# Kernel optimization log

Measured on AMD Instinct MI355X. Metric: run time of the kernel, lower is better.

Reference implementation:

```python
import jax, jax.numpy as jnp
import numpy as np
from jax import lax

S, B, VIN, VOUT, U, E = 64, 256, 128, 128, 1024, 512
START_CODE = 0
T_DEC = 25  # MAX_DECODE_STEPS


def gru_step(x, h, Wih, Whh, bih, bhh):
    # PyTorch GRU cell, gate order r,z,n
    gi = x @ Wih.T + bih
    gh = h @ Whh.T + bhh
    ir, iz, inn = jnp.split(gi, 3, axis=-1)
    hr, hz, hn = jnp.split(gh, 3, axis=-1)
    r = jax.nn.sigmoid(ir + hr)
    z = jax.nn.sigmoid(iz + hz)
    n = jnp.tanh(inn + r * hn)
    return (1.0 - z) * n + z * h


def setup_inputs() -> dict:
    key = jax.random.key(0)
    ks = jax.random.split(key, 20)
    sc = 0.05
    inp = {
        'x': jax.random.normal(ks[0], (S, B, VIN), jnp.float32),
        'x_len': jnp.maximum(jnp.sort(jax.random.randint(ks[1], (B,), 0, S + 1)), 1),
        'enc_Wih': jax.random.normal(ks[2], (3 * U, VIN), jnp.float32) * sc,
        'enc_Whh': jax.random.normal(ks[3], (3 * U, U), jnp.float32) * sc,
        'enc_bih': jnp.zeros((3 * U,), jnp.float32),
        'enc_bhh': jnp.zeros((3 * U,), jnp.float32),
        'dec_Wih': jax.random.normal(ks[4], (3 * U, E + U), jnp.float32) * sc,
        'dec_Whh': jax.random.normal(ks[5], (3 * U, U), jnp.float32) * sc,
        'dec_bih': jnp.zeros((3 * U,), jnp.float32),
        'dec_bhh': jnp.zeros((3 * U,), jnp.float32),
        'o2h_W': jax.random.normal(ks[6], (E, VOUT), jnp.float32) * sc,
        'o2h_b': jnp.zeros((E,), jnp.float32),
        'fc_W': jax.random.normal(ks[7], (VOUT, U), jnp.float32) * sc,
        'fc_b': jnp.zeros((VOUT,), jnp.float32),
        'W1_W': jax.random.normal(ks[8], (U, U), jnp.float32) * sc,
        'W1_b': jnp.zeros((U,), jnp.float32),
        'W2_W': jax.random.normal(ks[9], (U, U), jnp.float32) * sc,
        'W2_b': jnp.zeros((U,), jnp.float32),
        'V_W': jax.random.normal(ks[10], (1, U), jnp.float32) * sc,
        'V_b': jnp.zeros((1,), jnp.float32),
    }
    return inp


def _forward(x, x_len, enc_Wih, enc_Whh, enc_bih, enc_bhh,
             dec_Wih, dec_Whh, dec_bih, dec_bhh,
             o2h_W, o2h_b, fc_W, fc_b, W1_W, W1_b, W2_W, W2_b, V_W, V_b):
    # ---- Encoder GRU with length masking (pack/pad semantics) ----
    h0 = jnp.zeros((B, U), jnp.float32)
    t_idx = jnp.arange(S)

    def enc_step(h, inp_t):
        xt, t = inp_t
        mask = (t < x_len)[:, None]  # [B,1]
        hn = gru_step(xt, h, enc_Wih, enc_Whh, enc_bih, enc_bhh)
        h = jnp.where(mask, hn, h)
        out = jnp.where(mask, hn, 0.0)
        return h, out

    enc_hidden, enc_out = lax.scan(enc_step, h0, (x, t_idx))  # enc_out [S,B,U]
    enc_out = jnp.transpose(enc_out, (1, 0, 2))  # [B,S,U]

    # ---- Greedy decode (teacher_force=False), 25 steps ----
    enc_proj = enc_out @ W1_W.T + W1_b  # precompute W1(enc_output), [B,S,U]
    start = jnp.zeros((B, VOUT), jnp.float32).at[:, START_CODE].set(1.0)

    def dec_step(carry, _):
        h, dec_in = carry
        score = jnp.tanh(enc_proj + (h @ W2_W.T + W2_b)[:, None, :])  # [B,S,U]
        logits = score @ V_W.T + V_b  # [B,S,1]
        attn = jax.nn.softmax(logits, axis=1)
        ctx = jnp.sum(attn * enc_out, axis=1)  # [B,U]
        emb = dec_in @ o2h_W.T + o2h_b  # [B,E]
        gx = jnp.concatenate([ctx, emb], axis=-1)
        hn = gru_step(gx, h, dec_Wih, dec_Whh, dec_bih, dec_bhh)
        pred = hn @ fc_W.T + fc_b  # [B,VOUT]
        onehot = jax.nn.one_hot(jnp.argmax(pred, axis=-1), VOUT, dtype=pred.dtype)
        return (hn, lax.stop_gradient(onehot)), pred

    _, preds = lax.scan(dec_step, (enc_hidden, start), None, length=T_DEC - 1)
    return jnp.concatenate([start[None], preds], axis=0)  # [25,B,VOUT]


def reference(x, x_len, enc_Wih, enc_Whh, enc_bih, enc_bhh,
              dec_Wih, dec_Whh, dec_bih, dec_bhh,
              o2h_W, o2h_b, fc_W, fc_b, W1_W, W1_b, W2_W, W2_b, V_W, V_b):
    return _forward(x, x_len, enc_Wih, enc_Whh, enc_bih, enc_bhh,
                    dec_Wih, dec_Whh, dec_bih, dec_bhh,
                    o2h_W, o2h_b, fc_W, fc_b, W1_W, W1_b, W2_W, W2_b, V_W, V_b)
```

## Files before the change

### kernel.cpp

```cpp
#include <hip/hip_runtime.h>
#include <math.h>

#define SLEN 64
#define BATCH 256
#define VIND 128
#define VOUTD 128
#define UDIM 1024
#define EDIM 512
#define TDEC 25
#define GXW 1536
#define U3 3072
#define NSEG 12

typedef __attribute__((ext_vector_type(8))) short short8;
typedef __attribute__((ext_vector_type(4))) float f32x4;

#define MFMA(acc, A, B) acc = __builtin_amdgcn_mfma_f32_16x16x32_bf16((A), (B), (acc), 0, 0, 0)

__device__ __forceinline__ float sigm(float x) { return 1.f / (1.f + expf(-x)); }

__device__ __forceinline__ float tanhf_fast(float x) {
    float ax = fabsf(x);
    float e = __expf(-2.f * ax);
    float t = (1.f - e) / (1.f + e);
    return copysignf(t, x);
}

__device__ __forceinline__ short f2bf(float f) {
    unsigned u = __float_as_uint(f);
    u += 0x7FFF + ((u >> 16) & 1);
    return (short)(u >> 16);
}
__device__ __forceinline__ float bf2f(short h) {
    return __uint_as_float(((unsigned)(unsigned short)h) << 16);
}

__device__ __forceinline__ size_t pkChunk(int r, int k, int K) {
    return ((size_t)(r >> 4) * (K >> 5) + (k >> 5)) * 64 + ((r & 15) + 16 * ((k >> 3) & 3));
}

union S8 { short s[8]; short8 v; };

__device__ __forceinline__ void writeSplit8(short* Hi, short* Lo, size_t chunk,
                                            const float* vals) {
    S8 h, l;
#pragma unroll
    for (int j = 0; j < 8; j++) {
        short hb = f2bf(vals[j]);
        h.s[j] = hb;
        l.s[j] = f2bf(vals[j] - bf2f(hb));
    }
    ((short8*)Hi)[chunk] = h.v;
    ((short8*)Lo)[chunk] = l.v;
}

__global__ void init_kernel(float* __restrict__ h0, short* __restrict__ hpHi,
                            short* __restrict__ hpLo, float* __restrict__ out0,
                            int* __restrict__ idx,
                            const float* __restrict__ o2h_W,
                            const float* __restrict__ o2h_b,
                            float* __restrict__ o2hT) {
    int i = blockIdx.x * 256 + threadIdx.x;
    if (i < BATCH * UDIM) { h0[i] = 0.f; hpHi[i] = 0; hpLo[i] = 0; }
    if (i < BATCH * VOUTD) out0[i] = ((i & (VOUTD - 1)) == 0) ? 1.f : 0.f;
    if (i < BATCH) idx[i] = 0;
    if (i < VOUTD * EDIM) {
        int v = i >> 9, e = i & (EDIM - 1);
        o2hT[i] = o2h_W[(size_t)e * VOUTD + v] + o2h_b[e];
    }
}

struct PackSeg {
    const float* sA; const float* sB;
    short* Hi; short* Lo;
    int KA, KB, offA, offB, chunkStart;
};
struct PackArgs { PackSeg s[NSEG]; };

__global__ void pack_all(PackArgs pa, int total) {
    int gid = blockIdx.x * 256 + threadIdx.x;
    if (gid >= total) return;
    int si = 0;
#pragma unroll
    for (int i = 1; i < NSEG; i++) si = (gid >= pa.s[i].chunkStart) ? i : si;
    PackSeg sg = pa.s[si];
    int local = gid - sg.chunkStart;
    int K = sg.KA + sg.KB;
    int cpr = K >> 3;
    int r = local / cpr, k0 = (local - r * cpr) * 8;
    const float* src = (k0 < sg.KA)
        ? sg.sA + (size_t)(sg.offA + r) * sg.KA + k0
        : sg.sB + (size_t)(sg.offB + r) * sg.KB + (k0 - sg.KA);
    float v[8];
#pragma unroll
    for (int j = 0; j < 8; j++) v[j] = src[j];
    writeSplit8(sg.Hi, sg.Lo, pkChunk(r, k0, K), v);
}

__global__ __launch_bounds__(256) void gemm_w(
    const short8* __restrict__ Ahi, const short8* __restrict__ Alo,
    const short8* __restrict__ Whi, const short8* __restrict__ Wlo,
    const float* __restrict__ bias, float* __restrict__ C,
    int KT, int N) {
    int tid = threadIdx.x, lane = tid & 63, wave = tid >> 6;
    int m16 = blockIdx.x * 4 + (wave & 1) * 2;
    int nb = blockIdx.y * 8 + (wave >> 1) * 4;
    const short8* a0h = Ahi + (size_t)m16 * KT * 64 + lane;
    const short8* a1h = a0h + (size_t)KT * 64;
    const short8* a0l = Alo + (size_t)m16 * KT * 64 + lane;
    const short8* a1l = a0l + (size_t)KT * 64;
    const short8* w0h = Whi + (size_t)(nb + 0) * KT * 64 + lane;
    const short8* w1h = Whi + (size_t)(nb + 1) * KT * 64 + lane;
    const short8* w2h = Whi + (size_t)(nb + 2) * KT * 64 + lane;
    const short8* w3h = Whi + (size_t)(nb + 3) * KT * 64 + lane;
    const short8* w0l = Wlo + (size_t)(nb + 0) * KT * 64 + lane;
    const short8* w1l = Wlo + (size_t)(nb + 1) * KT * 64 + lane;
    const short8* w2l = Wlo + (size_t)(nb + 2) * KT * 64 + lane;
    const short8* w3l = Wlo + (size_t)(nb + 3) * KT * 64 + lane;
    f32x4 acc0[4] = {}, acc1[4] = {};

    for (int kt = 0; kt < KT; kt++) {
        size_t o = (size_t)kt * 64;
        short8 A0H = a0h[o], A1H = a1h[o], A0L = a0l[o], A1L = a1l[o];
        short8 WH0 = w0h[o], WL0 = w0l[o];
        MFMA(acc0[0], A0H, WH0); MFMA(acc1[0], A1H, WH0);
        MFMA(acc0[0], A0H, WL0); MFMA(acc1[0], A1H, WL0);
        MFMA(acc0[0], A0L, WH0); MFMA(acc1[0], A1L, WH0);
        short8 WH1 = w1h[o], WL1 = w1l[o];
        MFMA(acc0[1], A0H, WH1); MFMA(acc1[1], A1H, WH1);
        MFMA(acc0[1], A0H, WL1); MFMA(acc1[1], A1H, WL1);
        MFMA(acc0[1], A0L, WH1); MFMA(acc1[1], A1L, WH1);
        short8 WH2 = w2h[o], WL2 = w2l[o];
        MFMA(acc0[2], A0H, WH2); MFMA(acc1[2], A1H, WH2);
        MFMA(acc0[2], A0H, WL2); MFMA(acc1[2], A1H, WL2);
        MFMA(acc0[2], A0L, WH2); MFMA(acc1[2], A1L, WH2);
        short8 WH3 = w3h[o], WL3 = w3l[o];
        MFMA(acc0[3], A0H, WH3); MFMA(acc1[3], A1H, WH3);
        MFMA(acc0[3], A0H, WL3); MFMA(acc1[3], A1H, WL3);
        MFMA(acc0[3], A0L, WH3); MFMA(acc1[3], A1L, WH3);
    }
    int rsub = (lane >> 4) * 4, cn = lane & 15;
    int row0 = (m16 + 0) * 16 + rsub;
    int row1 = (m16 + 1) * 16 + rsub;
#pragma unroll
    for (int j = 0; j < 4; j++) {
        int col = (nb + j) * 16 + cn;
        float bb = bias ? bias[col] : 0.f;
#pragma unroll
        for (int r = 0; r < 4; r++) {
            C[(size_t)(row0 + r) * N + col] = acc0[j][r] + bb;
            C[(size_t)(row1 + r) * N + col] = acc1[j][r] + bb;
        }
    }
}

__global__ __launch_bounds__(256) void gemm_bm32(
    const short8* __restrict__ Ahi, const short8* __restrict__ Alo,
    const short8* __restrict__ Whi, const short8* __restrict__ Wlo,
    const float* __restrict__ bias, float* __restrict__ C,
    int KT, int N) {
    int tid = threadIdx.x, lane = tid & 63, wave = tid >> 6;
    int m16 = blockIdx.x * 2 + (wave & 1);
    int n16 = blockIdx.y * 4 + (wave >> 1) * 2;
    const short8* ah = Ahi + (size_t)m16 * KT * 64 + lane;
    const short8* al = Alo + (size_t)m16 * KT * 64 + lane;
    const short8* w0h = Whi + (size_t)n16 * KT * 64 + lane;
    const short8* w1h = w0h + (size_t)KT * 64;
    const short8* w0l = Wlo + (size_t)n16 * KT * 64 + lane;
    const short8* w1l = w0l + (size_t)KT * 64;
    f32x4 a0 = {0,0,0,0}, a1 = {0,0,0,0};
    for (int kt = 0; kt < KT; kt++) {
        size_t o = (size_t)kt * 64;
        short8 AH = ah[o], AL = al[o];
        short8 W0H = w0h[o], W0L = w0l[o], W1H = w1h[o], W1L = w1l[o];
        MFMA(a0, AH, W0H); MFMA(a1, AH, W1H);
        MFMA(a0, AH, W0L); MFMA(a1, AH, W1L);
        MFMA(a0, AL, W0H); MFMA(a1, AL, W1H);
    }
    int rsub = (lane >> 4) * 4, cn = lane & 15;
    float b0 = bias ? bias[(n16 + 0) * 16 + cn] : 0.f;
    float b1 = bias ? bias[(n16 + 1) * 16 + cn] : 0.f;
#pragma unroll
    for (int r = 0; r < 4; r++) {
        int row = m16 * 16 + rsub + r;
        C[(size_t)row * N + (n16 + 0) * 16 + cn] = a0[r] + b0;
        C[(size_t)row * N + (n16 + 1) * 16 + cn] = a1[r] + b1;
    }
}

__global__ __launch_bounds__(768) void enc_gru3(
    const short8* __restrict__ hinH8, const short8* __restrict__ hinL8,
    const short8* __restrict__ xH8, const short8* __restrict__ xL8,
    const short8* __restrict__ WihH, const short8* __restrict__ WihL,
    const short8* __restrict__ WrH, const short8* __restrict__ WrL,
    const short8* __restrict__ WzH, const short8* __restrict__ WzL,
    const short8* __restrict__ WnH, const short8* __restrict__ WnL,
    const float* __restrict__ bih, const float* __restrict__ bhh,
    const float* __restrict__ hinF, float* __restrict__ houtF,
    short* __restrict__ hoH, short* __restrict__ hoL,
    short* __restrict__ eaHi, short* __restrict__ eaLo,
    const int* __restrict__ x_len, int t) {
    __shared__ float sC[8][4][16][16];
    __shared__ float sHo[4][16][16];
    __shared__ float sEo[4][16][16];
    int tid = threadIdx.x, lane = tid & 63, wave = tid >> 6;
    int g = blockIdx.x;
    int m16a = blockIdx.y * 4;
    int gate = wave >> 2, hm = wave & 3, half = hm >> 1, mp = hm & 1;
    int t0 = mp * 2;
    const short8* a0h = hinH8 + (size_t)(m16a + t0) * 32 * 64 + (size_t)half * 16 * 64 + lane;
    const short8* a0l = hinL8 + (size_t)(m16a + t0) * 32 * 64 + (size_t)half * 16 * 64 + lane;
    const short8* a1h = a0h + (size_t)32 * 64;
    const short8* a1l = a0l + (size_t)32 * 64;
    const short8* WH0 = (gate == 0) ? WrH : (gate == 1) ? WzH : WnH;
    const short8* WL0 = (gate == 0) ? WrL : (gate == 1) ? WzL : WnL;
    const short8* wh = WH0 + (size_t)g * 32 * 64 + (size_t)half * 16 * 64 + lane;
    const short8* wl = WL0 + (size_t)g * 32 * 64 + (size_t)half * 16 * 64 + lane;
    const short8* x0h = xH8 + ((size_t)(t * 16 + m16a + t0) * 4 + half * 2) * 64 + lane;
    const short8* x0l = xL8 + ((size_t)(t * 16 + m16a + t0) * 4 + half * 2) * 64 + lane;
    const short8* x1h = x0h + (size_t)4 * 64;
    const short8* x1l = x0l + (size_t)4 * 64;
    const short8* wxh = WihH + ((size_t)(gate * 64 + g) * 4 + half * 2) * 64 + lane;
    const short8* wxl = WihL + ((size_t)(gate * 64 + g) * 4 + half * 2) * 64 + lane;

    f32x4 accA0 = {0, 0, 0, 0}, accA1 = {0, 0, 0, 0};
    for (int kt = 0; kt < 16; kt++) {
        size_t o = (size_t)kt * 64;
        short8 WH = wh[o], WL = wl[o];
        short8 A0H = a0h[o], A0L = a0l[o];
        MFMA(accA0, A0H, WH); MFMA(accA0, A0H, WL); MFMA(accA0, A0L, WH);
        short8 A1H = a1h[o], A1L = a1l[o];
        MFMA(accA1, A1H, WH); MFMA(accA1, A1H, WL); MFMA(accA1, A1L, WH);
    }
    f32x4 accX0 = {0, 0, 0, 0}, accX1 = {0, 0, 0, 0};
    if (gate < 2) {
#pragma unroll
        for (int kt = 0; kt < 2; kt++) {
            size_t o = (size_t)kt * 64;
            short8 WH = wxh[o], WL = wxl[o];
            short8 X0H = x0h[o], X0L = x0l[o];
            MFMA(accA0, X0H, WH); MFMA(accA0, X0H, WL); MFMA(accA0, X0L, WH);
            short8 X1H = x1h[o], X1L = x1l[o];
            MFMA(accA1, X1H, WH); MFMA(accA1, X1H, WL); MFMA(accA1, X1L, WH);
        }
    } else {
#pragma unroll
        for (int kt = 0; kt < 2; kt++) {
            size_t o = (size_t)kt * 64;
            short8 WH = wxh[o], WL = wxl[o];
            short8 X0H = x0h[o], X0L = x0l[o];
            MFMA(accX0, X0H, WH); MFMA(accX0, X0H, WL); MFMA(accX0, X0L, WH);
            short8 X1H = x1h[o], X1L = x1l[o];
            MFMA(accX1, X1H, WH); MFMA(accX1, X1H, WL); MFMA(accX1, X1L, WH);
        }
    }
    {
        int rsub = (lane >> 4) << 2, cn = lane & 15;
        if (gate < 2) {
            int slot = gate * 2 + half;
#pragma unroll
            for (int j = 0; j < 4; j++) {
                sC[slot][t0 + 0][rsub + j][cn] = accA0[j];
                sC[slot][t0 + 1][rsub + j][cn] = accA1[j];
            }
        } else {
#pragma unroll
            for (int j = 0; j < 4; j++) {
                sC[4 + half][t0 + 0][rsub + j][cn] = accA0[j];
                sC[4 + half][t0 + 1][rsub + j][cn] = accA1[j];
                sC[6 + half][t0 + 0][rsub + j][cn] = accX0[j];
                sC[6 + half][t0 + 1][rsub + j][cn] = accX1[j];
            }
        }
    }
    __syncthreads();
    if (wave < 4) {
        int tile = wave;
        int m16 = m16a + tile;
        int cu = g * 16 + (lane & 15);
        int rsub = (lane >> 4) << 2;
        float b_r = bih[cu] + bhh[cu];
        float b_z = bih[UDIM + cu] + bhh[UDIM + cu];
        float b_nh = bhh[2 * UDIM + cu];
        float b_ni = bih[2 * UDIM + cu];
#pragma unroll
        for (int j = 0; j < 4; j++) {
            int rr = rsub + j, cc = lane & 15;
            int b = m16 * 16 + rr;
            float rS = sC[0][tile][rr][cc] + sC[1][tile][rr][cc];
            float zS = sC[2][tile][rr][cc] + sC[3][tile][rr][cc];
            float nhS = sC[4][tile][rr][cc] + sC[5][tile][rr][cc];
            float niS = sC[6][tile][rr][cc] + sC[7][tile][rr][cc];
            float rg = sigm(rS + b_r);
            float zg = sigm(zS + b_z);
            float nn = tanhf(niS + b_ni + rg * (nhS + b_nh));
            float hp = hinF[(size_t)b * UDIM + cu];
            float hv = (1.f - zg) * nn + zg * hp;
            bool msk = t < x_len[b];
            float ho = msk ? hv : hp;
            houtF[(size_t)b * UDIM + cu] = ho;
            sHo[tile][rr][cc] = ho;
            sEo[tile][rr][cc] = msk ? hv : 0.f;
        }
    }
    __syncthreads();
    if (wave >= 4 && wave < 8 && lane < 32) {
        int tile = wave - 4;
        int m16 = m16a + tile;
        int rr = lane >> 1, oct = lane & 1;
        int brow = m16 * 16 + rr;
        int u0 = g * 16 + oct * 8;
        float v[8];
#pragma unroll
        for (int j = 0; j < 8; j++) v[j] = sHo[tile][rr][oct * 8 + j];
        writeSplit8(hoH, hoL, pkChunk(brow, u0, UDIM), v);
#pragma unroll
        for (int j = 0; j < 8; j++) v[j] = sEo[tile][rr][oct * 8 + j];
        writeSplit8(eaHi, eaLo, pkChunk(brow * SLEN + t, u0, UDIM), v);
    }
}

__global__ __launch_bounds__(768) void dec_gru3(
    const short8* __restrict__ hinH8, const short8* __restrict__ hinL8,
    const short8* __restrict__ gxH8, const short8* __restrict__ gxL8,
    const short8* __restrict__ WrH, const short8* __restrict__ WrL,
    const short8* __restrict__ WzH, const short8* __restrict__ WzL,
    const short8* __restrict__ WnhH, const short8* __restrict__ WnhL,
    const short8* __restrict__ WniH, const short8* __restrict__ WniL,
    const float* __restrict__ bih, const float* __restrict__ bhh,
    const float* __restrict__ hinF, float* __restrict__ houtF,
    short* __restrict__ hoH, short* __restrict__ hoL) {
    __shared__ float sC[8][4][16][16];
    __shared__ float sHo[4][16][16];
    int tid = threadIdx.x, lane = tid & 63, wave = tid >> 6;
    int g = blockIdx.x;
    int m16a = blockIdx.y * 4;
    int gate = wave >> 2, hm = wave & 3, half = hm >> 1, mp = hm & 1;
    int t0 = mp * 2;
    const short8* a0h = hinH8 + (size_t)(m16a + t0) * 32 * 64 + (size_t)half * 16 * 64 + lane;
    const short8* a0l = hinL8 + (size_t)(m16a + t0) * 32 * 64 + (size_t)half * 16 * 64 + lane;
    const short8* a1h = a0h + (size_t)32 * 64;
    const short8* a1l = a0l + (size_t)32 * 64;
    const short8* g0h = gxH8 + (size_t)(m16a + t0) * 48 * 64 + (size_t)half * 24 * 64 + lane;
    const short8* g0l = gxL8 + (size_t)(m16a + t0) * 48 * 64 + (size_t)half * 24 * 64 + lane;
    const short8* g1h = g0h + (size_t)48 * 64;
    const short8* g1l = g0l + (size_t)48 * 64;
    const short8 *whA, *wlA, *whB, *wlB;
    if (gate == 0) {
        whA = WrH + (size_t)g * 80 * 64 + (size_t)half * 16 * 64 + lane;
        wlA = WrL + (size_t)g * 80 * 64 + (size_t)half * 16 * 64 + lane;
        whB = WrH + (size_t)g * 80 * 64 + (size_t)(32 + half * 24) * 64 + lane;
        wlB = WrL + (size_t)g * 80 * 64 + (size_t)(32 + half * 24) * 64 + lane;
    } else if (gate == 1) {
        whA = WzH + (size_t)g * 80 * 64 + (size_t)half * 16 * 64 + lane;
        wlA = WzL + (size_t)g * 80 * 64 + (size_t)half * 16 * 64 + lane;
        whB = WzH + (size_t)g * 80 * 64 + (size_t)(32 + half * 24) * 64 + lane;
        wlB = WzL + (size_t)g * 80 * 64 + (size_t)(32 + half * 24) * 64 + lane;
    } else {
        whA = WnhH + (size_t)g * 32 * 64 + (size_t)half * 16 * 64 + lane;
        wlA = WnhL + (size_t)g * 32 * 64 + (size_t)half * 16 * 64 + lane;
        whB = WniH + (size_t)g * 48 * 64 + (size_t)half * 24 * 64 + lane;
        wlB = WniL + (size_t)g * 48 * 64 + (size_t)half * 24 * 64 + lane;
    }
    f32x4 accA0 = {0,0,0,0}, accA1 = {0,0,0,0};
    f32x4 accB0 = {0,0,0,0}, accB1 = {0,0,0,0};
    for (int kt = 0; kt < 16; kt++) {
        size_t o = (size_t)kt * 64;
        short8 WH = whA[o], WL = wlA[o];
        short8 A0H = a0h[o], A0L = a0l[o];
        MFMA(accA0, A0H, WH); MFMA(accA0, A0H, WL); MFMA(accA0, A0L, WH);
        short8 A1H = a1h[o], A1L = a1l[o];
        MFMA(accA1, A1H, WH); MFMA(accA1, A1H, WL); MFMA(accA1, A1L, WH);
    }
    for (int kt = 0; kt < 24; kt++) {
        size_t o = (size_t)kt * 64;
        short8 WH = whB[o], WL = wlB[o];
        short8 G0H = g0h[o], G0L = g0l[o];
        MFMA(accB0, G0H, WH); MFMA(accB0, G0H, WL); MFMA(accB0, G0L, WH);
        short8 G1H = g1h[o], G1L = g1l[o];
        MFMA(accB1, G1H, WH); MFMA(accB1, G1H, WL); MFMA(accB1, G1L, WH);
    }
    {
        int rsub = (lane >> 4) << 2, cn = lane & 15;
        if (gate < 2) {
            int slot = gate * 2 + half;
#pragma unroll
            for (int j = 0; j < 4; j++) {
                sC[slot][t0 + 0][rsub + j][cn] = accA0[j] + accB0[j];
                sC[slot][t0 + 1][rsub + j][cn] = accA1[j] + accB1[j];
            }
        } else {
#pragma unroll
            for (int j = 0; j < 4; j++) {
                sC[4 + half][t0 + 0][rsub + j][cn] = accA0[j];
                sC[4 + half][t0 + 1][rsub + j][cn] = accA1[j];
                sC[6 + half][t0 + 0][rsub + j][cn] = accB0[j];
                sC[6 + half][t0 + 1][rsub + j][cn] = accB1[j];
            }
        }
    }
    __syncthreads();
    if (wave < 4) {
        int tile = wave;
        int m16 = m16a + tile;
        int cu = g * 16 + (lane & 15);
        int rsub = (lane >> 4) << 2;
        float b_r = bih[cu] + bhh[cu];
        float b_z = bih[UDIM + cu] + bhh[UDIM + cu];
        float b_nh = bhh[2 * UDIM + cu];
        float b_ni = bih[2 * UDIM + cu];
#pragma unroll
        for (int j = 0; j < 4; j++) {
            int rr = rsub + j, cc = lane & 15;
            int b = m16 * 16 + rr;
            float rg = sigm(sC[0][tile][rr][cc] + sC[1][tile][rr][cc] + b_r);
            float zg = sigm(sC[2][tile][rr][cc] + sC[3][tile][rr][cc] + b_z);
            float nn = tanhf(sC[6][tile][rr][cc] + sC[7][tile][rr][cc] + b_ni +
                             rg * (sC[4][tile][rr][cc] + sC[5][tile][rr][cc] + b_nh));
            float hp = hinF[(size_t)b * UDIM + cu];
            float hv = (1.f - zg) * nn + zg * hp;
            houtF[(size_t)b * UDIM + cu] = hv;
            sHo[tile][rr][cc] = hv;
        }
    }
    __syncthreads();
    if (wave >= 4 && wave < 8 && lane < 32) {
        int tile = wave - 4;
        int m16 = m16a + tile;
        int rr = lane >> 1, oct = lane & 1;
        int brow = m16 * 16 + rr;
        int u0 = g * 16 + oct * 8;
        float v[8];
#pragma unroll
        for (int j = 0; j < 8; j++) v[j] = sHo[tile][rr][oct * 8 + j];
        writeSplit8(hoH, hoL, pkChunk(brow, u0, UDIM), v);
    }
}

__global__ __launch_bounds__(1024) void attn_ctx(
    const float* __restrict__ encProj,
    const short* __restrict__ eaHi, const short* __restrict__ eaLo,
    const float* __restrict__ tmp2, const float* __restrict__ V_W,
    const float* __restrict__ V_b,
    const float* __restrict__ o2hT,
    const int* __restrict__ idx, short* __restrict__ gxHi, short* __restrict__ gxLo) {
    int b = blockIdx.x;
    int tid = threadIdx.x, lane = tid & 63, wave = tid >> 6;
    __shared__ float s_t2[UDIM];
    __shared__ float s_v[UDIM];
    __shared__ float s_attn[SLEN];
    __shared__ float s_part[7][128][9];
    for (int u = tid; u < UDIM; u += 1024) {
        s_t2[u] = tmp2[(size_t)b * UDIM + u];
        s_v[u] = V_W[u];
    }
    __syncthreads();
    for (int s = wave; s < SLEN; s += 16) {
        const float4* ep4 = (const float4*)(encProj + ((size_t)b * SLEN + s) * UDIM);
        float p = 0.f;
        for (int u4 = lane; u4 < UDIM / 4; u4 += 64) {
            float4 e = ep4[u4];
            int u = 4 * u4;
            p += tanhf_fast(e.x + s_t2[u]) * s_v[u] +
                 tanhf_fast(e.y + s_t2[u + 1]) * s_v[u + 1] +
                 tanhf_fast(e.z + s_t2[u + 2]) * s_v[u + 2] +
                 tanhf_fast(e.w + s_t2[u + 3]) * s_v[u + 3];
        }
#pragma unroll
        for (int off = 32; off > 0; off >>= 1) p += __shfl_xor(p, off);
        if (lane == 0) s_attn[s] = p + V_b[0];
    }
    __syncthreads();
    if (tid < 64) {
        float v = s_attn[tid];
        float mx = v;
#pragma unroll
        for (int off = 32; off > 0; off >>= 1) mx = fmaxf(mx, __shfl_xor(mx, off));
        float e = expf(v - mx);
        float sum = e;
#pragma unroll
        for (int off = 32; off > 0; off >>= 1) sum += __shfl_xor(sum, off);
        s_attn[tid] = e / sum;
    }
    __syncthreads();
    {
        int grp = tid >> 7, tu = tid & 127;
        int u0 = tu * 8;
        float a[8] = {0, 0, 0, 0, 0, 0, 0, 0};
        const short8* hi8 = (const short8*)eaHi;
        const short8* lo8 = (const short8*)eaLo;
        int lanePart = 16 * ((u0 >> 3) & 3);
        int colPart = u0 >> 5;
        for (int s = grp * 8; s < grp * 8 + 8; s++) {
            int r = b * SLEN + s;
            size_t ch = ((size_t)(r >> 4) * (UDIM >> 5) + colPart) * 64 + (r & 15) + lanePart;
            S8 h, l;
            h.v = hi8[ch];
            l.v = lo8[ch];
            float w = s_attn[s];
#pragma unroll
            for (int j = 0; j < 8; j++) a[j] += w * (bf2f(h.s[j]) + bf2f(l.s[j]));
        }
        if (grp) {
#pragma unroll
            for (int j = 0; j < 8; j++) s_part[grp - 1][tu][j] = a[j];
        }
        __syncthreads();
        if (tid < 128) {
#pragma unroll
            for (int gg = 0; gg < 7; gg++)
#pragma unroll
                for (int j = 0; j < 8; j++) a[j] += s_part[gg][tu][j];
            writeSplit8(gxHi, gxLo, pkChunk(b, u0, GXW), a);
        } else if (tid < 192) {
            int e0 = (tid - 128) * 8;
            int ib = idx[b];
            const float* row = o2hT + (size_t)ib * EDIM + e0;
            float v[8];
#pragma unroll
            for (int j = 0; j < 8; j++) v[j] = row[j];
            writeSplit8(gxHi, gxLo, pkChunk(b, UDIM + e0, GXW), v);
        }
    }
}

__global__ __launch_bounds__(256) void fcw2(
    const short8* __restrict__ hHi, const short8* __restrict__ hLo,
    const short8* __restrict__ fcH, const short8* __restrict__ fcL,
    const float* __restrict__ fc_b, float* __restrict__ pred,
    int* __restrict__ idx,
    const short8* __restrict__ w2H, const short8* __restrict__ w2L,
    const float* __restrict__ W2_b, float* __restrict__ tmp2) {
    __shared__ float sP[16][129];
    int tid = threadIdx.x, lane = tid & 63, wave = tid >> 6;
    if (blockIdx.x < 16) {
        int fm = blockIdx.x;
        const short8* ah = hHi + (size_t)fm * 32 * 64 + lane;
        const short8* al = hLo + (size_t)fm * 32 * 64 + lane;
        int n0 = 2 * wave, n1 = 2 * wave + 1;
        const short8* w0h = fcH + (size_t)n0 * 32 * 64 + lane;
        const short8* w0l = fcL + (size_t)n0 * 32 * 64 + lane;
        const short8* w1h = fcH + (size_t)n1 * 32 * 64 + lane;
        const short8* w1l = fcL + (size_t)n1 * 32 * 64 + lane;
        f32x4 a0 = {0,0,0,0}, a1 = {0,0,0,0};
        for (int kt = 0; kt < 32; kt++) {
            size_t o = (size_t)kt * 64;
            short8 AH = ah[o], AL = al[o];
            short8 W0H = w0h[o], W0L = w0l[o], W1H = w1h[o], W1L = w1l[o];
            MFMA(a0, AH, W0H); MFMA(a1, AH, W1H);
            MFMA(a0, AH, W0L); MFMA(a1, AH, W1L);
            MFMA(a0, AL, W0H); MFMA(a1, AL, W1H);
        }
        int cn = lane & 15, rsub = (lane >> 4) << 2;
#pragma unroll
        for (int j = 0; j < 4; j++) {
            sP[rsub + j][n0 * 16 + cn] = a0[j] + fc_b[n0 * 16 + cn];
            sP[rsub + j][n1 * 16 + cn] = a1[j] + fc_b[n1 * 16 + cn];
        }
        __syncthreads();
        {
            int row = tid >> 4, c0 = (tid & 15) * 8;
            float* pr = pred + (size_t)(fm * 16 + row) * VOUTD;
#pragma unroll
            for (int j = 0; j < 8; j++) pr[c0 + j] = sP[row][c0 + j];
        }
        if (tid < 128) {
            int row = tid >> 3, seg = tid & 7;
            float v = -1e30f;
            int bi = 0;
            int c0 = seg * 16;
            for (int j = c0; j < c0 + 16; j++) {
                float w = sP[row][j];
                if (w > v) { v = w; bi = j; }
            }
#pragma unroll
            for (int off = 1; off < 8; off <<= 1) {
                float ov = __shfl_xor(v, off);
                int obi = __shfl_xor(bi, off);
                if (ov > v || (ov == v && obi < bi)) { v = ov; bi = obi; }
            }
            if (seg == 0) idx[fm * 16 + row] = bi;
        }
    } else {
        int lin = blockIdx.x - 16;
        int bx = lin & 7, by = lin >> 3;
        int m16 = bx * 2 + (wave & 1);
        int n16 = by * 4 + (wave >> 1) * 2;
        const short8* ah = hHi + (size_t)m16 * 32 * 64 + lane;
        const short8* al = hLo + (size_t)m16 * 32 * 64 + lane;
        const short8* w0h = w2H + (size_t)n16 * 32 * 64 + lane;
        const short8* w1h = w0h + (size_t)32 * 64;
        const short8* w0l = w2L + (size_t)n16 * 32 * 64 + lane;
        const short8* w1l = w0l + (size_t)32 * 64;
        f32x4 a0 = {0,0,0,0}, a1 = {0,0,0,0};
        for (int kt = 0; kt < 32; kt++) {
            size_t o = (size_t)kt * 64;
            short8 AH = ah[o], AL = al[o];
            short8 W0H = w0h[o], W0L = w0l[o], W1H = w1h[o], W1L = w1l[o];
            MFMA(a0, AH, W0H); MFMA(a1, AH, W1H);
            MFMA(a0, AH, W0L); MFMA(a1, AH, W1L);
            MFMA(a0, AL, W0H); MFMA(a1, AL, W1H);
        }
        int rsub = (lane >> 4) * 4, cn = lane & 15;
        float b0 = W2_b[(n16 + 0) * 16 + cn];
        float b1 = W2_b[(n16 + 1) * 16 + cn];
#pragma unroll
        for (int r = 0; r < 4; r++) {
            int row = m16 * 16 + rsub + r;
            tmp2[(size_t)row * UDIM + (n16 + 0) * 16 + cn] = a0[r] + b0;
            tmp2[(size_t)row * UDIM + (n16 + 1) * 16 + cn] = a1[r] + b1;
        }
    }
}

extern "C" void kernel_launch(void* const* d_in, const int* in_sizes, int n_in,
                              void* d_out, int out_size, void* d_ws, size_t ws_size,
                              hipStream_t stream) {
    const float* x       = (const float*)d_in[0];
    const int*   x_len   = (const int*)d_in[1];
    const float* enc_Wih = (const float*)d_in[2];
    const float* enc_Whh = (const float*)d_in[3];
    const float* enc_bih = (const float*)d_in[4];
    const float* enc_bhh = (const float*)d_in[5];
    const float* dec_Wih = (const float*)d_in[6];
    const float* dec_Whh = (const float*)d_in[7];
    const float* dec_bih = (const float*)d_in[8];
    const float* dec_bhh = (const float*)d_in[9];
    const float* o2h_W   = (const float*)d_in[10];
    const float* o2h_b   = (const float*)d_in[11];
    const float* fc_W    = (const float*)d_in[12];
    const float* fc_b    = (const float*)d_in[13];
    const float* W1_W    = (const float*)d_in[14];
    const float* W1_b    = (const float*)d_in[15];
    const float* W2_W    = (const float*)d_in[16];
    const float* W2_b    = (const float*)d_in[17];
    const float* V_W     = (const float*)d_in[18];
    const float* V_b     = (const float*)d_in[19];
    float* out = (float*)d_out;

    char* p = (char*)d_ws;
    auto alloc = [&](size_t bytes) -> char* {
        char* q = p;
        p += (bytes + 255) & ~(size_t)255;
        return q;
    };
    float* hAF  = (float*)alloc((size_t)BATCH * UDIM * 4);
    float* hBF  = (float*)alloc((size_t)BATCH * UDIM * 4);
    short* hAH  = (short*)alloc((size_t)BATCH * UDIM * 2);
    short* hAL  = (short*)alloc((size_t)BATCH * UDIM * 2);
    short* hBH  = (short*)alloc((size_t)BATCH * UDIM * 2);
    short* hBL  = (short*)alloc((size_t)BATCH * UDIM * 2);
    float* tmp2 = (float*)alloc((size_t)BATCH * UDIM * 4);
    short* gxHi = (short*)alloc((size_t)BATCH * GXW * 2);
    short* gxLo = (short*)alloc((size_t)BATCH * GXW * 2);
    short* encAHi = (short*)alloc((size_t)BATCH * SLEN * UDIM * 2);
    short* encALo = (short*)alloc((size_t)BATCH * SLEN * UDIM * 2);
    float* encProjF = (float*)alloc((size_t)BATCH * SLEN * UDIM * 4);
    short* eWihH = (short*)alloc((size_t)U3 * VIND * 2);
    short* eWihL = (short*)alloc((size_t)U3 * VIND * 2);
    short* eWrH = (short*)alloc((size_t)UDIM * UDIM * 2);
    short* eWrL = (short*)alloc((size_t)UDIM * UDIM * 2);
    short* eWzH = (short*)alloc((size_t)UDIM * UDIM * 2);
    short* eWzL = (short*)alloc((size_t)UDIM * UDIM * 2);
    short* eWnH = (short*)alloc((size_t)UDIM * UDIM * 2);
    short* eWnL = (short*)alloc((size_t)UDIM * UDIM * 2);
    short* dWrH = (short*)alloc((size_t)UDIM * 2560 * 2);
    short* dWrL = (short*)alloc((size_t)UDIM * 2560 * 2);
    short* dWzH = (short*)alloc((size_t)UDIM * 2560 * 2);
    short* dWzL = (short*)alloc((size_t)UDIM * 2560 * 2);
    short* dWnhH = (short*)alloc((size_t)UDIM * UDIM * 2);
    short* dWnhL = (short*)alloc((size_t)UDIM * UDIM * 2);
    short* dWniH = (short*)alloc((size_t)UDIM * GXW * 2);
    short* dWniL = (short*)alloc((size_t)UDIM * GXW * 2);
    short* w1Hi = (short*)alloc((size_t)UDIM * UDIM * 2);
    short* w1Lo = (short*)alloc((size_t)UDIM * UDIM * 2);
    short* w2Hi = (short*)alloc((size_t)UDIM * UDIM * 2);
    short* w2Lo = (short*)alloc((size_t)UDIM * UDIM * 2);
    short* fcHi = (short*)alloc((size_t)VOUTD * UDIM * 2);
    short* fcLo = (short*)alloc((size_t)VOUTD * UDIM * 2);
    short* xHi  = (short*)alloc((size_t)SLEN * BATCH * VIND * 2);
    short* xLo  = (short*)alloc((size_t)SLEN * BATCH * VIND * 2);
    int*   idx  = (int*)alloc(BATCH * 4);
    float* o2hT = (float*)alloc((size_t)VOUTD * EDIM * 4);

    init_kernel<<<(BATCH * UDIM + 255) / 256, 256, 0, stream>>>(
        hAF, hAH, hAL, out, idx, o2h_W, o2h_b, o2hT);

    {
        PackArgs pa;
        int cs = 0, n = 0;
        auto seg = [&](const float* sA, int KA, int offA, const float* sB, int KB,
                       int offB, short* Hi, short* Lo, int R) {
            pa.s[n] = {sA, sB, Hi, Lo, KA, KB, offA, offB, cs};
            cs += R * (KA + KB) / 8;
            n++;
        };
        seg(enc_Wih, VIND, 0, nullptr, 0, 0, eWihH, eWihL, U3);
        seg(enc_Whh, UDIM, 0, nullptr, 0, 0, eWrH, eWrL, UDIM);
        seg(enc_Whh, UDIM, UDIM, nullptr, 0, 0, eWzH, eWzL, UDIM);
        seg(enc_Whh, UDIM, 2 * UDIM, nullptr, 0, 0, eWnH, eWnL, UDIM);
        seg(dec_Whh, UDIM, 0, dec_Wih, GXW, 0, dWrH, dWrL, UDIM);
        seg(dec_Whh, UDIM, UDIM, dec_Wih, GXW, UDIM, dWzH, dWzL, UDIM);
        seg(dec_Whh, UDIM, 2 * UDIM, nullptr, 0, 0, dWnhH, dWnhL, UDIM);
        seg(dec_Wih, GXW, 2 * UDIM, nullptr, 0, 0, dWniH, dWniL, UDIM);
        seg(W1_W, UDIM, 0, nullptr, 0, 0, w1Hi, w1Lo, UDIM);
        seg(W2_W, UDIM, 0, nullptr, 0, 0, w2Hi, w2Lo, UDIM);
        seg(fc_W, UDIM, 0, nullptr, 0, 0, fcHi, fcLo, VOUTD);
        seg(x, VIND, 0, nullptr, 0, 0, xHi, xLo, SLEN * BATCH);
        pack_all<<<(cs + 255) / 256, 256, 0, stream>>>(pa, cs);
    }

    float* hcF = hAF; float* hnF = hBF;
    short *hcH = hAH, *hcL = hAL, *hnH = hBH, *hnL = hBL;
    for (int t = 0; t < SLEN; t++) {
        enc_gru3<<<dim3(64, 4), 768, 0, stream>>>(
            (const short8*)hcH, (const short8*)hcL,
            (const short8*)xHi, (const short8*)xLo,
            (const short8*)eWihH, (const short8*)eWihL,
            (const short8*)eWrH, (const short8*)eWrL,
            (const short8*)eWzH, (const short8*)eWzL,
            (const short8*)eWnH, (const short8*)eWnL,
            enc_bih, enc_bhh, hcF, hnF, hnH, hnL,
            encAHi, encALo, x_len, t);
        { float* tf = hcF; hcF = hnF; hnF = tf; }
        { short* th = hcH; hcH = hnH; hnH = th; th = hcL; hcL = hnL; hnL = th; }
    }

    gemm_w<<<dim3(SLEN * BATCH / 64, UDIM / 128), 256, 0, stream>>>(
        (const short8*)encAHi, (const short8*)encALo,
        (const short8*)w1Hi, (const short8*)w1Lo,
        W1_b, encProjF, UDIM / 32, UDIM);

    gemm_bm32<<<dim3(BATCH / 32, UDIM / 64), 256, 0, stream>>>(
        (const short8*)hcH, (const short8*)hcL,
        (const short8*)w2Hi, (const short8*)w2Lo,
        W2_b, tmp2, UDIM / 32, UDIM);

    for (int st = 0; st < TDEC - 1; st++) {
        attn_ctx<<<BATCH, 1024, 0, stream>>>(
            encProjF, encAHi, encALo, tmp2, V_W, V_b, o2hT, idx, gxHi, gxLo);
        dec_gru3<<<dim3(64, 4), 768, 0, stream>>>(
            (const short8*)hcH, (const short8*)hcL,
            (const short8*)gxHi, (const short8*)gxLo,
            (const short8*)dWrH, (const short8*)dWrL,
            (const short8*)dWzH, (const short8*)dWzL,
            (const short8*)dWnhH, (const short8*)dWnhL,
            (const short8*)dWniH, (const short8*)dWniL,
            dec_bih, dec_bhh, hcF, hnF, hnH, hnL);
        float* pred = out + (size_t)(1 + st) * BATCH * VOUTD;
        int nblk = (st == TDEC - 2) ? 16 : 144;
        fcw2<<<nblk, 256, 0, stream>>>(
            (const short8*)hnH, (const short8*)hnL,
            (const short8*)fcHi, (const short8*)fcLo,
            fc_b, pred, idx,
            (const short8*)w2Hi, (const short8*)w2Lo, W2_b, tmp2);
        { float* tf = hcF; hcF = hnF; hnF = tf; }
        { short* th = hcH; hcH = hnH; hnH = th; th = hcL; hcL = hnL; hnL = th; }
    }
}
```

Measured before the change: 3.352 ms.

## Overlap decoder hidden-state GEMM with attention in one fused launch

Merges the attention/context kernel with the hidden-state half of the decoder GRU GEMM (h·Whh for the r, z and n gates) into one launch. Blocks below BATCH do attention, and the remaining blocks compute the hidden-side gate products into a new global buffer. The finishing kernel then computes only the input-side (gx) GEMM and adds the stored partial sums. The aim is to run the h-dependent matmul alongside attention instead of after it, at the cost of an extra 6×B×U float round-trip through global memory. Blocks that run both roles also carry attention's shared-memory footprint, which can limit occupancy.

New measurement: 3.676 ms. 9.6% more time.

```diff
diff --git a/kernel.cpp b/kernel.cpp
--- a/kernel.cpp
+++ b/kernel.cpp
@@ -320,13 +320,147 @@
     }
 }
 
-__global__ __launch_bounds__(768) void dec_gru3(
+__global__ __launch_bounds__(1024, 8) void attn_dech(
+    const float* __restrict__ encProj,
+    const short* __restrict__ eaHi, const short* __restrict__ eaLo,
+    const float* __restrict__ tmp2, const float* __restrict__ V_W,
+    const float* __restrict__ V_b,
+    const float* __restrict__ o2hT,
+    const int* __restrict__ idx, short* __restrict__ gxHi, short* __restrict__ gxLo,
     const short8* __restrict__ hinH8, const short8* __restrict__ hinL8,
+    const short8* __restrict__ WrH, const short8* __restrict__ WrL,
+    const short8* __restrict__ WzH, const short8* __restrict__ WzL,
+    const short8* __restrict__ WnhH, const short8* __restrict__ WnhL,
+    float* __restrict__ ghA) {
+    int tid = threadIdx.x, lane = tid & 63, wave = tid >> 6;
+    if (blockIdx.x < BATCH) {
+        int b = blockIdx.x;
+        __shared__ float s_t2[UDIM];
+        __shared__ float s_v[UDIM];
+        __shared__ float s_attn[SLEN];
+        __shared__ float s_part[7][128][9];
+        for (int u = tid; u < UDIM; u += 1024) {
+            s_t2[u] = tmp2[(size_t)b * UDIM + u];
+            s_v[u] = V_W[u];
+        }
+        __syncthreads();
+        for (int s = wave; s < SLEN; s += 16) {
+            const float4* ep4 = (const float4*)(encProj + ((size_t)b * SLEN + s) * UDIM);
+            float p = 0.f;
+            for (int u4 = lane; u4 < UDIM / 4; u4 += 64) {
+                float4 e = ep4[u4];
+                int u = 4 * u4;
+                p += tanhf_fast(e.x + s_t2[u]) * s_v[u] +
+                     tanhf_fast(e.y + s_t2[u + 1]) * s_v[u + 1] +
+                     tanhf_fast(e.z + s_t2[u + 2]) * s_v[u + 2] +
+                     tanhf_fast(e.w + s_t2[u + 3]) * s_v[u + 3];
+            }
+#pragma unroll
+            for (int off = 32; off > 0; off >>= 1) p += __shfl_xor(p, off);
+            if (lane == 0) s_attn[s] = p + V_b[0];
+        }
+        __syncthreads();
+        if (tid < 64) {
+            float v = s_attn[tid];
+            float mx = v;
+#pragma unroll
+            for (int off = 32; off > 0; off >>= 1) mx = fmaxf(mx, __shfl_xor(mx, off));
+            float e = expf(v - mx);
+            float sum = e;
+#pragma unroll
+            for (int off = 32; off > 0; off >>= 1) sum += __shfl_xor(sum, off);
+            s_attn[tid] = e / sum;
+        }
+        __syncthreads();
+        {
+            int grp = tid >> 7, tu = tid & 127;
+            int u0 = tu * 8;
+            float a[8] = {0, 0, 0, 0, 0, 0, 0, 0};
+            const short8* hi8 = (const short8*)eaHi;
+            const short8* lo8 = (const short8*)eaLo;
+            int lanePart = 16 * ((u0 >> 3) & 3);
+            int colPart = u0 >> 5;
+            for (int s = grp * 8; s < grp * 8 + 8; s++) {
+                int r = b * SLEN + s;
+                size_t ch = ((size_t)(r >> 4) * (UDIM >> 5) + colPart) * 64 + (r & 15) + lanePart;
+                S8 h, l;
+                h.v = hi8[ch];
+                l.v = lo8[ch];
+                float w = s_attn[s];
+#pragma unroll
+                for (int j = 0; j < 8; j++) a[j] += w * (bf2f(h.s[j]) + bf2f(l.s[j]));
+            }
+            if (grp) {
+#pragma unroll
+                for (int j = 0; j < 8; j++) s_part[grp - 1][tu][j] = a[j];
+            }
+            __syncthreads();
+            if (tid < 128) {
+#pragma unroll
+                for (int gg = 0; gg < 7; gg++)
+#pragma unroll
+                    for (int j = 0; j < 8; j++) a[j] += s_part[gg][tu][j];
+                writeSplit8(gxHi, gxLo, pkChunk(b, u0, GXW), a);
+            } else if (tid < 192) {
+                int e0 = (tid - 128) * 8;
+                int ib = idx[b];
+                const float* row = o2hT + (size_t)ib * EDIM + e0;
+                float v[8];
+#pragma unroll
+                for (int j = 0; j < 8; j++) v[j] = row[j];
+                writeSplit8(gxHi, gxLo, pkChunk(b, UDIM + e0, GXW), v);
+            }
+        }
+    } else if (wave < 12) {
+        int lin = blockIdx.x - BATCH;
+        int g = lin & 63, mq = lin >> 6;
+        int m16a = mq * 4;
+        int gate = wave >> 2, hm = wave & 3, half = hm >> 1, mp = hm & 1;
+        int t0 = mp * 2;
+        const short8* a0h = hinH8 + (size_t)(m16a + t0) * 32 * 64 + (size_t)half * 16 * 64 + lane;
+        const short8* a0l = hinL8 + (size_t)(m16a + t0) * 32 * 64 + (size_t)half * 16 * 64 + lane;
+        const short8* a1h = a0h + (size_t)32 * 64;
+        const short8* a1l = a0l + (size_t)32 * 64;
+        const short8 *whA, *wlA;
+        if (gate == 0) {
+            whA = WrH + (size_t)g * 80 * 64 + (size_t)half * 16 * 64 + lane;
+            wlA = WrL + (size_t)g * 80 * 64 + (size_t)half * 16 * 64 + lane;
+        } else if (gate == 1) {
+            whA = WzH + (size_t)g * 80 * 64 + (size_t)half * 16 * 64 + lane;
+            wlA = WzL + (size_t)g * 80 * 64 + (size_t)half * 16 * 64 + lane;
+        } else {
+            whA = WnhH + (size_t)g * 32 * 64 + (size_t)half * 16 * 64 + lane;
+            wlA = WnhL + (size_t)g * 32 * 64 + (size_t)half * 16 * 64 + lane;
+        }
+        f32x4 accA0 = {0,0,0,0}, accA1 = {0,0,0,0};
+        for (int kt = 0; kt < 16; kt++) {
+            size_t o = (size_t)kt * 64;
+            short8 WH = whA[o], WL = wlA[o];
+            short8 A0H = a0h[o], A0L = a0l[o];
+            MFMA(accA0, A0H, WH); MFMA(accA0, A0H, WL); MFMA(accA0, A0L, WH);
+            short8 A1H = a1h[o], A1L = a1l[o];
+            MFMA(accA1, A1H, WH); MFMA(accA1, A1H, WL); MFMA(accA1, A1L, WH);
+        }
+        int slot = gate * 2 + half;
+        int rsub = (lane >> 4) << 2, cn = lane & 15;
+        int cu = g * 16 + cn;
+        float* base = ghA + (size_t)slot * BATCH * UDIM;
+#pragma unroll
+        for (int j = 0; j < 4; j++) {
+            int r0 = (m16a + t0) * 16 + rsub + j;
+            int r1 = (m16a + t0 + 1) * 16 + rsub + j;
+            base[(size_t)r0 * UDIM + cu] = accA0[j];
+            base[(size_t)r1 * UDIM + cu] = accA1[j];
+        }
+    }
+}
+
+__global__ __launch_bounds__(768) void dec_fin(
     const short8* __restrict__ gxH8, const short8* __restrict__ gxL8,
     const short8* __restrict__ WrH, const short8* __restrict__ WrL,
     const short8* __restrict__ WzH, const short8* __restrict__ WzL,
-    const short8* __restrict__ WnhH, const short8* __restrict__ WnhL,
     const short8* __restrict__ WniH, const short8* __restrict__ WniL,
+    const float* __restrict__ ghA,
     const float* __restrict__ bih, const float* __restrict__ bhh,
     const float* __restrict__ hinF, float* __restrict__ houtF,
     short* __restrict__ hoH, short* __restrict__ hoL) {
@@ -337,41 +471,22 @@
     int m16a = blockIdx.y * 4;
     int gate = wave >> 2, hm = wave & 3, half = hm >> 1, mp = hm & 1;
     int t0 = mp * 2;
-    const short8* a0h = hinH8 + (size_t)(m16a + t0) * 32 * 64 + (size_t)half * 16 * 64 + lane;
-    const short8* a0l = hinL8 + (size_t)(m16a + t0) * 32 * 64 + (size_t)half * 16 * 64 + lane;
-    const short8* a1h = a0h + (size_t)32 * 64;
-    const short8* a1l = a0l + (size_t)32 * 64;
     const short8* g0h = gxH8 + (size_t)(m16a + t0) * 48 * 64 + (size_t)half * 24 * 64 + lane;
     const short8* g0l = gxL8 + (size_t)(m16a + t0) * 48 * 64 + (size_t)half * 24 * 64 + lane;
     const short8* g1h = g0h + (size_t)48 * 64;
     const short8* g1l = g0l + (size_t)48 * 64;
-    const short8 *whA, *wlA, *whB, *wlB;
+    const short8 *whB, *wlB;
     if (gate == 0) {
-        whA = WrH + (size_t)g * 80 * 64 + (size_t)half * 16 * 64 + lane;
-        wlA = WrL + (size_t)g * 80 * 64 + (size_t)half * 16 * 64 + lane;
         whB = WrH + (size_t)g * 80 * 64 + (size_t)(32 + half * 24) * 64 + lane;
         wlB = WrL + (size_t)g * 80 * 64 + (size_t)(32 + half * 24) * 64 + lane;
     } else if (gate == 1) {
-        whA = WzH + (size_t)g * 80 * 64 + (size_t)half * 16 * 64 + lane;
-        wlA = WzL + (size_t)g * 80 * 64 + (size_t)half * 16 * 64 + lane;
         whB = WzH + (size_t)g * 80 * 64 + (size_t)(32 + half * 24) * 64 + lane;
         wlB = WzL + (size_t)g * 80 * 64 + (size_t)(32 + half * 24) * 64 + lane;
     } else {
-        whA = WnhH + (size_t)g * 32 * 64 + (size_t)half * 16 * 64 + lane;
-        wlA = WnhL + (size_t)g * 32 * 64 + (size_t)half * 16 * 64 + lane;
         whB = WniH + (size_t)g * 48 * 64 + (size_t)half * 24 * 64 + lane;
         wlB = WniL + (size_t)g * 48 * 64 + (size_t)half * 24 * 64 + lane;
     }
-    f32x4 accA0 = {0,0,0,0}, accA1 = {0,0,0,0};
     f32x4 accB0 = {0,0,0,0}, accB1 = {0,0,0,0};
-    for (int kt = 0; kt < 16; kt++) {
-        size_t o = (size_t)kt * 64;
-        short8 WH = whA[o], WL = wlA[o];
-        short8 A0H = a0h[o], A0L = a0l[o];
-        MFMA(accA0, A0H, WH); MFMA(accA0, A0H, WL); MFMA(accA0, A0L, WH);
-        short8 A1H = a1h[o], A1L = a1l[o];
-        MFMA(accA1, A1H, WH); MFMA(accA1, A1H, WL); MFMA(accA1, A1L, WH);
-    }
     for (int kt = 0; kt < 24; kt++) {
         size_t o = (size_t)kt * 64;
         short8 WH = whB[o], WL = wlB[o];
@@ -381,19 +496,25 @@
         MFMA(accB1, G1H, WH); MFMA(accB1, G1H, WL); MFMA(accB1, G1L, WH);
     }
     {
+        int slot = gate * 2 + half;
         int rsub = (lane >> 4) << 2, cn = lane & 15;
+        int cu = g * 16 + cn;
+        const float* base = ghA + (size_t)slot * BATCH * UDIM;
         if (gate < 2) {
-            int slot = gate * 2 + half;
 #pragma unroll
             for (int j = 0; j < 4; j++) {
-                sC[slot][t0 + 0][rsub + j][cn] = accA0[j] + accB0[j];
-                sC[slot][t0 + 1][rsub + j][cn] = accA1[j] + accB1[j];
+                int r0 = (m16a + t0) * 16 + rsub + j;
+                int r1 = (m16a + t0 + 1) * 16 + rsub + j;
+                sC[slot][t0 + 0][rsub + j][cn] = base[(size_t)r0 * UDIM + cu] + accB0[j];
+                sC[slot][t0 + 1][rsub + j][cn] = base[(size_t)r1 * UDIM + cu] + accB1[j];
             }
         } else {
 #pragma unroll
             for (int j = 0; j < 4; j++) {
-                sC[4 + half][t0 + 0][rsub + j][cn] = accA0[j];
-                sC[4 + half][t0 + 1][rsub + j][cn] = accA1[j];
+                int r0 = (m16a + t0) * 16 + rsub + j;
+                int r1 = (m16a + t0 + 1) * 16 + rsub + j;
+                sC[4 + half][t0 + 0][rsub + j][cn] = base[(size_t)r0 * UDIM + cu];
+                sC[4 + half][t0 + 1][rsub + j][cn] = base[(size_t)r1 * UDIM + cu];
                 sC[6 + half][t0 + 0][rsub + j][cn] = accB0[j];
                 sC[6 + half][t0 + 1][rsub + j][cn] = accB1[j];
             }
@@ -434,93 +555,6 @@
 #pragma unroll
         for (int j = 0; j < 8; j++) v[j] = sHo[tile][rr][oct * 8 + j];
         writeSplit8(hoH, hoL, pkChunk(brow, u0, UDIM), v);
-    }
-}
-
-__global__ __launch_bounds__(1024) void attn_ctx(
-    const float* __restrict__ encProj,
-    const short* __restrict__ eaHi, const short* __restrict__ eaLo,
-    const float* __restrict__ tmp2, const float* __restrict__ V_W,
-    const float* __restrict__ V_b,
-    const float* __restrict__ o2hT,
-    const int* __restrict__ idx, short* __restrict__ gxHi, short* __restrict__ gxLo) {
-    int b = blockIdx.x;
-    int tid = threadIdx.x, lane = tid & 63, wave = tid >> 6;
-    __shared__ float s_t2[UDIM];
-    __shared__ float s_v[UDIM];
-    __shared__ float s_attn[SLEN];
-    __shared__ float s_part[7][128][9];
-    for (int u = tid; u < UDIM; u += 1024) {
-        s_t2[u] = tmp2[(size_t)b * UDIM + u];
-        s_v[u] = V_W[u];
-    }
-    __syncthreads();
-    for (int s = wave; s < SLEN; s += 16) {
-        const float4* ep4 = (const float4*)(encProj + ((size_t)b * SLEN + s) * UDIM);
-        float p = 0.f;
-        for (int u4 = lane; u4 < UDIM / 4; u4 += 64) {
-            float4 e = ep4[u4];
-            int u = 4 * u4;
-            p += tanhf_fast(e.x + s_t2[u]) * s_v[u] +
-                 tanhf_fast(e.y + s_t2[u + 1]) * s_v[u + 1] +
-                 tanhf_fast(e.z + s_t2[u + 2]) * s_v[u + 2] +
-                 tanhf_fast(e.w + s_t2[u + 3]) * s_v[u + 3];
-        }
-#pragma unroll
-        for (int off = 32; off > 0; off >>= 1) p += __shfl_xor(p, off);
-        if (lane == 0) s_attn[s] = p + V_b[0];
-    }
-    __syncthreads();
-    if (tid < 64) {
-        float v = s_attn[tid];
-        float mx = v;
-#pragma unroll
-        for (int off = 32; off > 0; off >>= 1) mx = fmaxf(mx, __shfl_xor(mx, off));
-        float e = expf(v - mx);
-        float sum = e;
-#pragma unroll
-        for (int off = 32; off > 0; off >>= 1) sum += __shfl_xor(sum, off);
-        s_attn[tid] = e / sum;
-    }
-    __syncthreads();
-    {
-        int grp = tid >> 7, tu = tid & 127;
-        int u0 = tu * 8;
-        float a[8] = {0, 0, 0, 0, 0, 0, 0, 0};
-        const short8* hi8 = (const short8*)eaHi;
-        const short8* lo8 = (const short8*)eaLo;
-        int lanePart = 16 * ((u0 >> 3) & 3);
-        int colPart = u0 >> 5;
-        for (int s = grp * 8; s < grp * 8 + 8; s++) {
-            int r = b * SLEN + s;
-            size_t ch = ((size_t)(r >> 4) * (UDIM >> 5) + colPart) * 64 + (r & 15) + lanePart;
-            S8 h, l;
-            h.v = hi8[ch];
-            l.v = lo8[ch];
-            float w = s_attn[s];
-#pragma unroll
-            for (int j = 0; j < 8; j++) a[j] += w * (bf2f(h.s[j]) + bf2f(l.s[j]));
-        }
-        if (grp) {
-#pragma unroll
-            for (int j = 0; j < 8; j++) s_part[grp - 1][tu][j] = a[j];
-        }
-        __syncthreads();
-        if (tid < 128) {
-#pragma unroll
-            for (int gg = 0; gg < 7; gg++)
-#pragma unroll
-                for (int j = 0; j < 8; j++) a[j] += s_part[gg][tu][j];
-            writeSplit8(gxHi, gxLo, pkChunk(b, u0, GXW), a);
-        } else if (tid < 192) {
-            int e0 = (tid - 128) * 8;
-            int ib = idx[b];
-            const float* row = o2hT + (size_t)ib * EDIM + e0;
-            float v[8];
-#pragma unroll
-            for (int j = 0; j < 8; j++) v[j] = row[j];
-            writeSplit8(gxHi, gxLo, pkChunk(b, UDIM + e0, GXW), v);
-        }
     }
 }
 
@@ -656,6 +690,7 @@
     short* encAHi = (short*)alloc((size_t)BATCH * SLEN * UDIM * 2);
     short* encALo = (short*)alloc((size_t)BATCH * SLEN * UDIM * 2);
     float* encProjF = (float*)alloc((size_t)BATCH * SLEN * UDIM * 4);
+    float* ghA  = (float*)alloc((size_t)6 * BATCH * UDIM * 4);
     short* eWihH = (short*)alloc((size_t)U3 * VIND * 2);
     short* eWihL = (short*)alloc((size_t)U3 * VIND * 2);
     short* eWrH = (short*)alloc((size_t)UDIM * UDIM * 2);
@@ -737,16 +772,19 @@
         W2_b, tmp2, UDIM / 32, UDIM);
 
     for (int st = 0; st < TDEC - 1; st++) {
-        attn_ctx<<<BATCH, 1024, 0, stream>>>(
-            encProjF, encAHi, encALo, tmp2, V_W, V_b, o2hT, idx, gxHi, gxLo);
-        dec_gru3<<<dim3(64, 4), 768, 0, stream>>>(
+        attn_dech<<<2 * BATCH, 1024, 0, stream>>>(
+            encProjF, encAHi, encALo, tmp2, V_W, V_b, o2hT, idx, gxHi, gxLo,
             (const short8*)hcH, (const short8*)hcL,
+            (const short8*)dWrH, (const short8*)dWrL,
+            (const short8*)dWzH, (const short8*)dWzL,
+            (const short8*)dWnhH, (const short8*)dWnhL,
+            ghA);
+        dec_fin<<<dim3(64, 4), 768, 0, stream>>>(
             (const short8*)gxHi, (const short8*)gxLo,
             (const short8*)dWrH, (const short8*)dWrL,
             (const short8*)dWzH, (const short8*)dWzL,
-            (const short8*)dWnhH, (const short8*)dWnhL,
             (const short8*)dWniH, (const short8*)dWniL,
-            dec_bih, dec_bhh, hcF, hnF, hnH, hnL);
+            ghA, dec_bih, dec_bhh, hcF, hnF, hnH, hnL);
         float* pred = out + (size_t)(1 + st) * BATCH * VOUTD;
         int nblk = (st == TDEC - 2) ? 16 : 144;
         fcw2<<<nblk, 256, 0, stream>>>(
```
